# Kernel optimization log

Measured on AMD Instinct MI355X. Metric: run time of the kernel, lower is better.

## Reference

```python
import jax, jax.numpy as jnp
import numpy as np

DIM, HEADS, DH, CHUNK, DEPTH = 1024, 8, 128, 64, 2
BATCH, SEQLEN = 2, 4096
MAX_LR = 0.01
EPS = 1e-6


def _rmsnorm(x, g=None):
    y = x * jax.lax.rsqrt(jnp.mean(x * x, axis=-1, keepdims=True) + EPS)
    return y * g if g is not None else y


def _mem_mlp(ws, x):
    # MemoryMLP: x @ W0, then silu before each subsequent layer
    x = x @ ws[0]
    for w in ws[1:]:
        x = jax.nn.silu(x) @ w
    return x


def _assoc_scan(gates, x):
    # y_t = gates_t * y_{t-1} + x_t along axis 3 (chunk axis)
    g = jnp.broadcast_to(gates, x.shape)
    def op(a, b):
        ga, xa = a
        gb, xb = b
        return ga * gb, gb * xa + xb
    _, y = jax.lax.associative_scan(op, (g, x), axis=3)
    return y


def setup_inputs() -> dict:
    key = jax.random.key(0)
    ks = jax.random.split(key, 12)
    b, n, d, h, dh = BATCH, SEQLEN, DIM, HEADS, DH
    di = h * dh
    lin = lambda k, i, o: jax.random.normal(k, (i, o), jnp.float32) * np.float32(1.0 / np.sqrt(i))
    return {
        "seq": jax.random.normal(ks[0], (b, n, d), jnp.float32),
        "store_norm_g": jnp.ones((d,), jnp.float32),
        "retrieve_norm_g": jnp.ones((d,), jnp.float32),
        "w_kv": lin(ks[1], d, 2 * di),
        "w_q": lin(ks[2], d, di),
        "w_step": lin(ks[3], d, h),
        "w_mom": lin(ks[4], d, h),
        "w_decay": lin(ks[5], d, h),
        "w_gate": lin(ks[6], d, h),
        "w_combine": lin(ks[7], di, d),
        "mh_gamma": jnp.zeros((h, 1, dh), jnp.float32),
        "mem_w0": lin(ks[8], dh, dh),
        "mem_w1": lin(ks[9], dh, dh),
    }


def reference(seq, store_norm_g, retrieve_norm_g, w_kv, w_q, w_step, w_mom,
              w_decay, w_gate, w_combine, mh_gamma, mem_w0, mem_w1):
    b, n, d = seq.shape
    h, dh, c = HEADS, DH, CHUNK
    nc = n // c
    mem_ws = (mem_w0, mem_w1)

    # ---------------- store memories (chunked test-time training) ----------------
    ss = _rmsnorm(seq, store_norm_g)                                    # (b,n,d)
    lr = jax.nn.sigmoid(jnp.einsum('bnd,dh->bhn', ss, w_step)) * MAX_LR  # adaptive step
    lr = lr.reshape(b, h, nc, c)
    cmean = ss.reshape(b, nc, c, d).mean(axis=2)                        # chunk mean-reduce
    mom_gate = jax.nn.sigmoid(jnp.einsum('bnd,dh->bhn', cmean, w_mom))   # (b,h,nc)
    decay = jax.nn.sigmoid(jnp.einsum('bnd,dh->bhn', cmean, w_decay))    # (b,h,nc)

    kv = ss @ w_kv                                                      # (b,n,2*h*dh)
    keys, values = jnp.split(kv, 2, axis=-1)
    split = lambda t: t.reshape(b, n, h, dh).transpose(0, 2, 1, 3).reshape(b, h, nc, c, dh)
    keys, values = split(keys), split(values)

    # per-chunk grad of weighted mse wrt memory MLP weights (vmap(grad), as in torch.func)
    def chunk_loss(ws, k, lrc, v):
        pred = _mem_mlp(ws, k)                                          # (c,dh)
        return jnp.sum(jnp.mean((pred - v) ** 2, axis=-1) * lrc)
    flat = lambda t: t.reshape(b * h * nc, c, dh)
    grads = jax.vmap(jax.grad(chunk_loss), in_axes=(None, 0, 0, 0))(
        mem_ws, flat(keys), lr.reshape(b * h * nc, c), flat(values))
    grads = jnp.stack([g.reshape(b, h, nc, dh, dh) for g in grads])     # (depth,b,h,nc,dh,dh)
    surprise = -grads

    gm = mom_gate[None, :, :, :, None, None]
    gd = (1.0 - decay)[None, :, :, :, None, None]
    momentum = _assoc_scan(gm, surprise)                                # momentum scan over chunks
    updates = _assoc_scan(gd, momentum)                                 # decayed cumulative weight deltas

    # ---------------- retrieve memories ----------------
    sr = _rmsnorm(seq, retrieve_norm_g)
    sr = jnp.pad(sr[:, c - 1:], ((0, 0), (0, c - 1), (0, 0)))           # causal shift by chunk-1
    q = (sr @ w_q).reshape(b, n, h, dh).transpose(0, 2, 1, 3).reshape(b, h, nc, c, dh)

    w0 = mem_w0 + updates[0]                                            # (b,h,nc,dh,dh)
    w1 = mem_w1 + updates[1]
    x = jnp.einsum('bhncd,bhnde->bhnce', q, w0)
    vals = jnp.einsum('bhncd,bhnde->bhnce', jax.nn.silu(x), w1)         # (b,h,nc,c,dh)
    vals = vals.reshape(b, h, n, dh)

    vals = _rmsnorm(vals) * (mh_gamma + 1.0)                            # multihead rmsnorm
    gate = jax.nn.sigmoid(jnp.einsum('bnd,dh->bhn', sr, w_gate))[..., None]
    vals = vals * gate                                                  # retrieve gate (heads>1)
    vals = vals.transpose(0, 2, 1, 3).reshape(b, n, h * dh)             # merge heads
    out = vals @ w_combine                                              # combine heads
    out = jnp.pad(out, ((0, 0), (c - 1, 0), (0, 0)))[:, :n]             # restore alignment
    return out
```

## Files before the change

### kernel.cpp

```cpp
#include <hip/hip_runtime.h>
#include <stdint.h>


#define SEQ 4096
#define NTOK 8192

typedef unsigned short u16;
typedef __attribute__((ext_vector_type(8))) short short8;
typedef __attribute__((ext_vector_type(4))) float f32x4;
typedef __attribute__((ext_vector_type(2))) unsigned int u32x2;

__device__ __forceinline__ u16 f2b(float f) {
  union { float f; uint32_t u; } c; c.f = f;
  uint32_t u = c.u;
  uint32_t r = (u + 0x7fffu + ((u >> 16) & 1u)) >> 16;
  return (u16)r;
}
__device__ __forceinline__ float b2f(u16 h) {
  union { uint32_t u; float f; } c; c.u = ((uint32_t)h) << 16;
  return c.f;
}
__device__ __forceinline__ float sigm(float x) { return 1.f / (1.f + __expf(-x)); }
__device__ __forceinline__ uint32_t pk2(float a, float b) {
  return (uint32_t)f2b(a) | ((uint32_t)f2b(b) << 16);
}
__device__ __forceinline__ void gl16(const void* g, void* l) {
  __builtin_amdgcn_global_load_lds(
      (const __attribute__((address_space(1))) unsigned int*)g,
      (__attribute__((address_space(3))) unsigned int*)l, 16, 0, 0);
}

__device__ __forceinline__ int sidx(int r, int c) {
  return r*128 + ((((c>>3) ^ (r&7))<<3) | (c&7));
}
__device__ __forceinline__ short8 frag_row_lds128(const u16* buf, int row, int ks, int l4) {
  int g = ks*4 + l4;
  return *(const short8*)&buf[row*128 + ((g ^ (row&7))<<3)];
}
__device__ __forceinline__ short8 frag_tile(const u16* t, int row, int ks, int l4) {
  return *(const short8*)&t[row*64 + (((ks*4 + l4) ^ (row&7))<<3)];
}
__device__ __forceinline__ int taddr(int c, int r0) {
  return c*64 + (r0 ^ ((c&7)<<3));
}


__global__ __launch_bounds__(256) void transpose_bf16(
    const float* __restrict__ src, u16* __restrict__ dst, int R, int C)
{
  __shared__ u16 tile[64*66];
  int tiles_x = C >> 6;
  int tx = blockIdx.x % tiles_x, ty = blockIdx.x / tiles_x;
  int c0 = tx*64, r0 = ty*64;
#pragma unroll
  for (int it=0; it<16; ++it) {
    int idx = it*256 + threadIdx.x;
    int rr = idx>>6, cc = idx&63;
    tile[cc*66 + rr] = f2b(src[(size_t)(r0+rr)*C + c0+cc]);
  }
  __syncthreads();
#pragma unroll
  for (int it=0; it<16; ++it) {
    int idx = it*256 + threadIdx.x;
    int rr = idx>>6, cc = idx&63;
    dst[(size_t)(c0+rr)*R + r0+cc] = tile[rr*66 + cc];
  }
}

__global__ __launch_bounds__(256) void smallprep(
    const float* __restrict__ w0, const float* __restrict__ w1,
    u16* __restrict__ w0Ts, u16* __restrict__ w1Ts, u16* __restrict__ w1bs)
{
  int id = blockIdx.x*256 + threadIdx.x;
  int i = id>>7, j = id&127;
  float a = w0[id], b = w1[id];
  w0Ts[sidx(j,i)] = f2b(a);
  w1Ts[sidx(j,i)] = f2b(b);
  w1bs[sidx(i,j)] = f2b(b);
}


__global__ __launch_bounds__(256) void norms_kernel(
    const float* __restrict__ seq, const float* __restrict__ gs,
    const float* __restrict__ gr, const float* __restrict__ wstep,
    const float* __restrict__ wgate, u16* __restrict__ ss,
    u16* __restrict__ sr, float* __restrict__ lr, float* __restrict__ gate)
{
  int t = blockIdx.x; int b = t>>12, pos = t&4095;
  int tid = threadIdx.x;
  const float* row = seq + (size_t)t*1024;
  float x[4]; float ssq = 0.f;
#pragma unroll
  for (int i=0;i<4;++i){ x[i]=row[i*256+tid]; ssq += x[i]*x[i]; }
  for (int m=32;m;m>>=1) ssq += __shfl_xor(ssq, m);
  __shared__ float red[4];
  __shared__ float r2[4][16];
  int wv = tid>>6;
  if ((tid&63)==0) red[wv] = ssq;
  __syncthreads();
  float tot = red[0]+red[1]+red[2]+red[3];
  float inv = rsqrtf(tot*(1.f/1024.f) + 1e-6f);
  float ps[8], pg[8];
#pragma unroll
  for (int h=0;h<8;++h){ ps[h]=0.f; pg[h]=0.f; }
#pragma unroll
  for (int i=0;i<4;++i) {
    int d = i*256+tid;
    float sv = x[i]*inv*gs[d];
    float rv = x[i]*inv*gr[d];
    ss[(size_t)t*1024+d] = f2b(sv);
    sr[(size_t)t*1024+d] = f2b(rv);
#pragma unroll
    for (int h=0;h<8;++h) { ps[h] += sv*wstep[d*8+h]; pg[h] += rv*wgate[d*8+h]; }
  }
#pragma unroll
  for (int h=0;h<8;++h)
    for (int m=32;m;m>>=1){ ps[h] += __shfl_xor(ps[h],m); pg[h] += __shfl_xor(pg[h],m); }
  if ((tid&63)==0) {
#pragma unroll
    for (int h=0;h<8;++h){ r2[wv][h]=ps[h]; r2[wv][8+h]=pg[h]; }
  }
  __syncthreads();
  if (tid < 16) {
    float s = r2[0][tid]+r2[1][tid]+r2[2][tid]+r2[3][tid];
    float sg = sigm(s);
    if (tid<8) lr[((size_t)(b*8+tid))*4096 + pos] = sg*0.01f;
    else gate[((size_t)(b*8+(tid-8)))*4096 + pos] = sg;
  }
}


__global__ __launch_bounds__(256) void chunkgates_kernel(
    const u16* __restrict__ ss, const float* __restrict__ wmom,
    const float* __restrict__ wdec, float* __restrict__ mg,
    float* __restrict__ d1m)
{
  int bc = blockIdx.x; int b = bc>>6, ch = bc&63;
  size_t t0 = (size_t)(b*4096 + ch*64)*1024;
  int tid = threadIdx.x;
  float cm[4]; cm[0]=cm[1]=cm[2]=cm[3]=0.f;
  for (int tok=0; tok<64; ++tok) {
#pragma unroll
    for (int i=0;i<4;++i)
      cm[i] += b2f(ss[t0 + (size_t)tok*1024 + i*256 + tid]);
  }
  float pm[8], pd[8];
#pragma unroll
  for (int h=0;h<8;++h){ pm[h]=0.f; pd[h]=0.f; }
#pragma unroll
  for (int i=0;i<4;++i) {
    float v = cm[i]*(1.f/64.f);
    int d = i*256+tid;
#pragma unroll
    for (int h=0;h<8;++h){ pm[h]+=v*wmom[d*8+h]; pd[h]+=v*wdec[d*8+h]; }
  }
#pragma unroll
  for (int h=0;h<8;++h)
    for (int m=32;m;m>>=1){ pm[h] += __shfl_xor(pm[h],m); pd[h] += __shfl_xor(pd[h],m); }
  __shared__ float r2[4][16];
  int wv = tid>>6;
  if ((tid&63)==0) {
#pragma unroll
    for (int h=0;h<8;++h){ r2[wv][h]=pm[h]; r2[wv][8+h]=pd[h]; }
  }
  __syncthreads();
  if (tid < 16) {
    float s = r2[0][tid]+r2[1][tid]+r2[2][tid]+r2[3][tid];
    if (tid<8) mg[(b*8+tid)*64 + ch] = sigm(s);
    else d1m[(b*8+(tid-8))*64 + ch] = 1.f - sigm(s);
  }
}


__global__ __launch_bounds__(512, 4) void gemm_bt(
    const u16* __restrict__ A, const u16* __restrict__ Bt,
    void* __restrict__ C, int M, int N, int K, int out_f32,
    u16* __restrict__ kvT)
{
  __shared__ __align__(16) u16 As[2][128*64];
  __shared__ __align__(16) u16 Bs[2][128*64];
  int tid = threadIdx.x;
  int w = tid>>6, lane = tid&63;
  int wr = w>>2, wc = w&3;
  int l15 = lane&15, l4 = lane>>4;
  int rl = lane>>3;
  int cg = (lane&7) ^ rl;
  int nwg = gridDim.x*gridDim.y;
  int wg  = blockIdx.y*gridDim.x + blockIdx.x;
  int cpx = nwg >> 3;
  int swz = (wg & 7)*cpx + (wg >> 3);
  int bx = swz % gridDim.x, by = swz / gridDim.x;
  int brow = by*128, bcol = bx*128;
  f32x4 acc[4][2] = {};

  auto STAGE = [&](int buf, int kt) {
#pragma unroll
    for (int i=0;i<2;++i) {
      int row = w*16 + i*8;
      gl16(&A [(size_t)(brow+row+rl)*K + kt + cg*8], &As[buf][row*64]);
      gl16(&Bt[(size_t)(bcol+row+rl)*K + kt + cg*8], &Bs[buf][row*64]);
    }
  };

  int nk = K >> 6;
  STAGE(0, 0);
  asm volatile("s_waitcnt vmcnt(0)");
  __syncthreads();
  for (int t=0; t<nk; ++t) {
    int cur = t & 1;
    if (t+1 < nk) STAGE(cur^1, (t+1)*64);
#pragma unroll
    for (int ks=0; ks<2; ++ks) {
      short8 af[4], bf[2];
#pragma unroll
      for (int m=0;m<4;++m) {
        int row = wr*64 + m*16 + l15;
        int g = ks*4 + l4;
        af[m] = *(const short8*)&As[cur][row*64 + ((g ^ (row&7))<<3)];
      }
#pragma unroll
      for (int n=0;n<2;++n) {
        int row = wc*32 + n*16 + l15;
        int g = ks*4 + l4;
        bf[n] = *(const short8*)&Bs[cur][row*64 + ((g ^ (row&7))<<3)];
      }
#pragma unroll
      for (int m=0;m<4;++m)
#pragma unroll
        for (int n=0;n<2;++n)
          acc[m][n] = __builtin_amdgcn_mfma_f32_16x16x32_bf16(af[m], bf[n], acc[m][n], 0,0,0);
    }
    asm volatile("s_waitcnt vmcnt(0)");
    __syncthreads();
  }
#pragma unroll
  for (int m=0;m<4;++m) {
#pragma unroll
    for (int n=0;n<2;++n) {
      int col = bcol + wc*32 + n*16 + l15;
#pragma unroll
      for (int j=0;j<4;++j) {
        int row = brow + wr*64 + m*16 + l4*4 + j;
        if (out_f32) ((float*)C)[(size_t)row*N + col] = acc[m][n][j];
        else ((u16*)C)[(size_t)row*N + col] = f2b(acc[m][n][j]);
      }
    }
  }
  if (kvT) {
#pragma unroll
    for (int m=0;m<4;++m) {
#pragma unroll
      for (int n=0;n<2;++n) {
        int col = bcol + wc*32 + n*16 + l15;
        if (col < 1024) {
          int row0 = brow + wr*64 + m*16 + l4*4;
          int d = col & 127;
          int chunk = ((row0>>12)*8 + (col>>7))*64 + ((row0&4095)>>6);
          int rr = row0 & 63;
          u32x2 p; p[0] = pk2(acc[m][n][0], acc[m][n][1]);
                   p[1] = pk2(acc[m][n][2], acc[m][n][3]);
          *(u32x2*)&kvT[(size_t)chunk*8192 + taddr(d, rr)] = p;
        }
      }
    }
  }
}


__global__ __launch_bounds__(512) void mlp_fwd(
    const u16* __restrict__ kvout, const float* __restrict__ lr,
    const u16* __restrict__ w0Ts, const u16* __restrict__ w1Ts,
    const u16* __restrict__ w1bs,
    u16* __restrict__ aTg, u16* __restrict__ dpTg, u16* __restrict__ dxTg)
{
  __shared__ __align__(16) u16 W0L[16384];
  __shared__ __align__(16) u16 W1L[16384];
  __shared__ __align__(16) u16 WBL[16384];
  __shared__ __align__(16) u16 abuf[16384];
  int tid = threadIdx.x;
  int w = tid>>6, lane = tid&63;
  int l15 = lane&15, l4 = lane>>4;
#pragma unroll
  for (int it=0; it<4; ++it) {
    int wb = it*512 + w*64;
    gl16((const short8*)w0Ts + wb + lane, (short8*)W0L + wb);
    gl16((const short8*)w1Ts + wb + lane, (short8*)W1L + wb);
    gl16((const short8*)w1bs + wb + lane, (short8*)WBL + wb);
  }
  __syncthreads();
  u16* ab = abuf + w*2048;
  int r0 = l4*4;
  int q = w&3, half = w>>2;
  int rb = q*16;
#pragma unroll
  for (int it2=0; it2<2; ++it2) {
    int cidx = blockIdx.x*4 + it2*2 + half;
    int bh = cidx>>6, ch = cidx&63;
    int b = bh>>3, hh = bh&7;
    size_t t0 = (size_t)(b*4096 + ch*64 + rb);
    size_t tout = (size_t)cidx*8192;
    f32x4 lrv = *(const f32x4*)&lr[(size_t)bh*4096 + ch*64 + rb + r0];

    f32x4 x1[8] = {};
#pragma unroll
    for (int ks=0; ks<4; ++ks) {
      short8 af = *(const short8*)&kvout[(t0 + l15)*2048 + hh*128 + ks*32 + l4*8];
#pragma unroll
      for (int n=0;n<8;++n) {
        short8 bf = frag_row_lds128(W0L, n*16+l15, ks, l4);
        x1[n] = __builtin_amdgcn_mfma_f32_16x16x32_bf16(af, bf, x1[n], 0,0,0);
      }
    }
#pragma unroll
    for (int n=0;n<8;++n) {
      int c = n*16 + l15;
      float av[4];
#pragma unroll
      for (int j=0;j<4;++j){ float xv = x1[n][j]; av[j] = xv*sigm(xv); }
      ab[sidx(r0+0,c)] = f2b(av[0]);
      ab[sidx(r0+1,c)] = f2b(av[1]);
      ab[sidx(r0+2,c)] = f2b(av[2]);
      ab[sidx(r0+3,c)] = f2b(av[3]);
      u32x2 p; p[0] = pk2(av[0],av[1]); p[1] = pk2(av[2],av[3]);
      *(u32x2*)&aTg[tout + taddr(c, rb + r0)] = p;
    }
    f32x4 pr[8] = {};
#pragma unroll
    for (int ks=0; ks<4; ++ks) {
      short8 af = frag_row_lds128(ab, l15, ks, l4);
#pragma unroll
      for (int n=0;n<8;++n) {
        short8 bf = frag_row_lds128(W1L, n*16+l15, ks, l4);
        pr[n] = __builtin_amdgcn_mfma_f32_16x16x32_bf16(af, bf, pr[n], 0,0,0);
      }
    }
#pragma unroll
    for (int n=0;n<8;++n) {
      int c = n*16 + l15;
      float dv[4];
#pragma unroll
      for (int j=0;j<4;++j) {
        float vv = b2f(kvout[(t0+r0+j)*2048 + 1024 + hh*128 + c]);
        dv[j] = 0.015625f * lrv[j] * (pr[n][j] - vv);
      }
      ab[sidx(r0+0,c)] = f2b(dv[0]);
      ab[sidx(r0+1,c)] = f2b(dv[1]);
      ab[sidx(r0+2,c)] = f2b(dv[2]);
      ab[sidx(r0+3,c)] = f2b(dv[3]);
      u32x2 p; p[0] = pk2(dv[0],dv[1]); p[1] = pk2(dv[2],dv[3]);
      *(u32x2*)&dpTg[tout + taddr(c, rb + r0)] = p;
    }
    f32x4 da[8] = {};
#pragma unroll
    for (int ks=0; ks<4; ++ks) {
      short8 af = frag_row_lds128(ab, l15, ks, l4);
#pragma unroll
      for (int n=0;n<8;++n) {
        short8 bf = frag_row_lds128(WBL, n*16+l15, ks, l4);
        da[n] = __builtin_amdgcn_mfma_f32_16x16x32_bf16(af, bf, da[n], 0,0,0);
      }
    }
#pragma unroll
    for (int n=0;n<8;++n) {
      int c = n*16 + l15;
      float d[4];
#pragma unroll
      for (int j=0;j<4;++j) {
        float xv = x1[n][j];
        float sg = sigm(xv);
        d[j] = da[n][j]*(sg*(1.f + xv*(1.f - sg)));
      }
      u32x2 p; p[0] = pk2(d[0],d[1]); p[1] = pk2(d[2],d[3]);
      *(u32x2*)&dxTg[tout + taddr(c, rb + r0)] = p;
    }
  }
}


__global__ __launch_bounds__(256) void grad_op(
    const u16* __restrict__ dpT, const u16* __restrict__ aT,
    const u16* __restrict__ dxT, const u16* __restrict__ kT,
    u16* __restrict__ S)
{
  __shared__ __align__(16) u16 lds[16384];
  int bid = blockIdx.x;
  int op = bid >> 10;
  int sub = bid & 1023, bh = sub>>6, ch = sub&63;
  size_t tin = (size_t)sub*8192;
  const u16* Ain = op ? (dxT + tin) : (dpT + tin);
  const u16* Bin = op ? (kT  + tin) : (aT  + tin);
  int tid = threadIdx.x;
  int w = tid>>6, lane = tid&63;
  int l15 = lane&15, l4 = lane>>4;

#pragma unroll
  for (int it=0; it<4; ++it) {
    int wb = it*256 + w*64;
    gl16((const short8*)Ain + wb + lane, (short8*)lds + wb);
    gl16((const short8*)Bin + wb + lane, (short8*)(lds+8192) + wb);
  }
  __syncthreads();

  f32x4 g[2][8] = {};
#pragma unroll
  for (int ks=0; ks<2; ++ks) {
    short8 af[2];
#pragma unroll
    for (int mi=0; mi<2; ++mi)
      af[mi] = frag_tile(lds, w*32 + mi*16 + l15, ks, l4);
#pragma unroll
    for (int n=0;n<8;++n) {
      short8 bf = frag_tile(lds+8192, n*16 + l15, ks, l4);
#pragma unroll
      for (int mi=0;mi<2;++mi)
        g[mi][n] = __builtin_amdgcn_mfma_f32_16x16x32_bf16(af[mi], bf, g[mi][n], 0,0,0);
    }
  }
  __syncthreads();

#pragma unroll
  for (int mi=0;mi<2;++mi)
#pragma unroll
    for (int n=0;n<8;++n)
#pragma unroll
      for (int j=0;j<4;++j) {
        int m = w*32 + mi*16 + l4*4 + j, c = n*16 + l15;
        lds[sidx(m,c)] = f2b(-g[mi][n][j]);
      }
  __syncthreads();

  u16* Sout = S + ((size_t)((op ? bh : 16+bh))*64 + ch)*16384;
#pragma unroll
  for (int it=0; it<8; ++it)
    ((short8*)Sout)[it*256+tid] = ((const short8*)lds)[it*256+tid];
}


__global__ __launch_bounds__(256) void scan_kernel(
    u16* __restrict__ S, const float* __restrict__ mg, const float* __restrict__ d1m,
    const u16* __restrict__ w0Ts, const u16* __restrict__ w1Ts)
{
  int bidx = blockIdx.x;
  int eblk = bidx & 63;
  int mbh = bidx >> 6;
  int bh = mbh & 15;
  int e = eblk*256 + threadIdx.x;
  u16* base = S + (size_t)mbh*64*16384 + e;
  float wv = b2f(((mbh < 16) ? w0Ts : w1Ts)[e]);
  const float* g1 = mg + bh*64;
  const float* g2 = d1m + bh*64;
  float mom = 0.f, upd = 0.f;
  for (int c2=0; c2<64; ++c2) {
    float s = b2f(base[(size_t)c2*16384]);
    mom = g1[c2]*mom + s;
    upd = g2[c2]*upd + mom;
    base[(size_t)c2*16384] = f2b(wv + upd);
  }
}


__global__ __launch_bounds__(256) void retrieve_kernel(
    const u16* __restrict__ qn, const u16* __restrict__ W,
    const float* __restrict__ gamma, const float* __restrict__ gate,
    u16* __restrict__ vals)
{
  __shared__ __align__(16) u16 W0s[16384];
  __shared__ __align__(16) u16 W1s[16384];
  __shared__ __align__(16) u16 QA[8192];
  int bid = blockIdx.x;
  int bh = bid>>6, ch = bid&63;
  int b = bh>>3, h = bh&7;
  int tid = threadIdx.x;
  int w = tid>>6, lane = tid&63;
  int l15 = lane&15, l4 = lane>>4;
  const u16* W0g = W + ((size_t)bh*64 + ch)*16384;
  const u16* W1g = W + ((size_t)(16+bh)*64 + ch)*16384;
#pragma unroll
  for (int it=0; it<8; ++it) {
    int wb = it*256 + w*64;
    gl16((const short8*)W0g + wb + lane, (short8*)W0s + wb);
    gl16((const short8*)W1g + wb + lane, (short8*)W1s + wb);
  }
  u16* qa = QA + w*2048;
#pragma unroll
  for (int it=0; it<4; ++it) {
    int task = it*64 + lane;
    int rloc = task>>4, g = task&15;
    int posn = ch*64 + w*16 + rloc + 63;
    short8 v;
    if (posn < 4096) v = *(const short8*)&qn[((size_t)(b*4096+posn))*1024 + h*128 + g*8];
    else {
#pragma unroll
      for (int i=0;i<8;++i) v[i]=0;
    }
    *(short8*)&qa[rloc*128 + ((g ^ (rloc&7))<<3)] = v;
  }
  __syncthreads();
  f32x4 xx[8] = {};
#pragma unroll
  for (int ks=0; ks<4; ++ks) {
    short8 af = frag_row_lds128(qa, l15, ks, l4);
#pragma unroll
    for (int n=0;n<8;++n) {
      short8 bf = frag_row_lds128(W0s, n*16+l15, ks, l4);
      xx[n] = __builtin_amdgcn_mfma_f32_16x16x32_bf16(af, bf, xx[n], 0,0,0);
    }
  }
  int r0 = l4*4;
#pragma unroll
  for (int n=0;n<8;++n) {
    int c = n*16 + l15;
#pragma unroll
    for (int j=0;j<4;++j) {
      float xv = xx[n][j];
      qa[sidx(r0+j,c)] = f2b(xv * sigm(xv));
    }
  }
  f32x4 vv[8] = {};
#pragma unroll
  for (int ks=0; ks<4; ++ks) {
    short8 af = frag_row_lds128(qa, l15, ks, l4);
#pragma unroll
    for (int n=0;n<8;++n) {
      short8 bf = frag_row_lds128(W1s, n*16+l15, ks, l4);
      vv[n] = __builtin_amdgcn_mfma_f32_16x16x32_bf16(af, bf, vv[n], 0,0,0);
    }
  }
#pragma unroll
  for (int j=0;j<4;++j) {
    float ssq = 0.f;
#pragma unroll
    for (int n=0;n<8;++n) ssq += vv[n][j]*vv[n][j];
    ssq += __shfl_xor(ssq,1); ssq += __shfl_xor(ssq,2);
    ssq += __shfl_xor(ssq,4); ssq += __shfl_xor(ssq,8);
    float rms = rsqrtf(ssq*(1.f/128.f) + 1e-6f);
    int posn = ch*64 + w*16 + r0 + j + 63;
    if (posn < 4096) {
      float gt = gate[(size_t)bh*4096 + posn];
      size_t orow = ((size_t)(b*4096+posn))*1024 + h*128;
#pragma unroll
      for (int n=0;n<8;++n) {
        int c = n*16 + l15;
        vals[orow + c] = f2b(vv[n][j]*rms*(1.f + gamma[h*128+c])*gt);
      }
    }
  }
}

extern "C" void kernel_launch(void* const* d_in, const int* in_sizes, int n_in,
                              void* d_out, int out_size, void* d_ws, size_t ws_size,
                              hipStream_t stream) {
  const float* seq    = (const float*)d_in[0];
  const float* gstore = (const float*)d_in[1];
  const float* gret   = (const float*)d_in[2];
  const float* wkv    = (const float*)d_in[3];
  const float* wq     = (const float*)d_in[4];
  const float* wstep  = (const float*)d_in[5];
  const float* wmom   = (const float*)d_in[6];
  const float* wdec   = (const float*)d_in[7];
  const float* wgate  = (const float*)d_in[8];
  const float* wcomb  = (const float*)d_in[9];
  const float* gamma  = (const float*)d_in[10];
  const float* w0f    = (const float*)d_in[11];
  const float* w1f    = (const float*)d_in[12];
  float* out = (float*)d_out;
  (void)in_sizes; (void)n_in; (void)out_size; (void)ws_size;

  char* p = (char*)d_ws;
  size_t off = 0;
  auto alloc = [&](size_t bytes) -> void* {
    void* r = p + off; off += (bytes + 255) & ~(size_t)255; return r;
  };
  u16* wkvT   = (u16*)alloc((size_t)2048*1024*2);
  u16* wqT    = (u16*)alloc((size_t)1024*1024*2);
  u16* wcombT = (u16*)alloc((size_t)1024*1024*2);
  u16* w0Ts   = (u16*)alloc(16384*2);
  u16* w1Ts   = (u16*)alloc(16384*2);
  u16* w1bs   = (u16*)alloc(16384*2);
  u16* ss     = (u16*)alloc((size_t)NTOK*1024*2);
  u16* sr     = (u16*)alloc((size_t)NTOK*1024*2);
  u16* kvout  = (u16*)alloc((size_t)NTOK*2048*2);
  u16* qn     = (u16*)alloc((size_t)NTOK*1024*2);
  u16* vals   = (u16*)alloc((size_t)NTOK*1024*2);
  float* lr   = (float*)alloc((size_t)16*4096*4);
  float* gate = (float*)alloc((size_t)16*4096*4);
  float* mg   = (float*)alloc(1024*4);
  float* d1m  = (float*)alloc(1024*4);
  u16* S      = (u16*)alloc((size_t)32*64*16384*2);
  u16* kTg    = (u16*)alloc((size_t)1024*8192*2);
  u16* aTg    = (u16*)alloc((size_t)1024*8192*2);
  u16* dpTg   = (u16*)alloc((size_t)1024*8192*2);
  u16* dxTg   = (u16*)alloc((size_t)1024*8192*2);

  transpose_bf16<<<dim3(512),dim3(256),0,stream>>>(wkv, wkvT, 1024, 2048);
  transpose_bf16<<<dim3(256),dim3(256),0,stream>>>(wq, wqT, 1024, 1024);
  transpose_bf16<<<dim3(256),dim3(256),0,stream>>>(wcomb, wcombT, 1024, 1024);
  smallprep<<<dim3(64),dim3(256),0,stream>>>(w0f, w1f, w0Ts, w1Ts, w1bs);
  norms_kernel<<<dim3(NTOK),dim3(256),0,stream>>>(seq, gstore, gret, wstep, wgate, ss, sr, lr, gate);
  chunkgates_kernel<<<dim3(128),dim3(256),0,stream>>>(ss, wmom, wdec, mg, d1m);
  gemm_bt<<<dim3(16,64),dim3(512),0,stream>>>(ss, wkvT, kvout, 8192, 2048, 1024, 0, kTg);
  gemm_bt<<<dim3(8,64),dim3(512),0,stream>>>(sr, wqT, qn, 8192, 1024, 1024, 0, nullptr);
  mlp_fwd<<<dim3(256),dim3(512),0,stream>>>(kvout, lr, w0Ts, w1Ts, w1bs, aTg, dpTg, dxTg);
  grad_op<<<dim3(2048),dim3(256),0,stream>>>(dpTg, aTg, dxTg, kTg, S);
  scan_kernel<<<dim3(2048),dim3(256),0,stream>>>(S, mg, d1m, w0Ts, w1Ts);
  hipMemsetAsync(vals, 0, 63*1024*2, stream);
  hipMemsetAsync(vals + (size_t)4096*1024, 0, 63*1024*2, stream);
  retrieve_kernel<<<dim3(1024),dim3(256),0,stream>>>(qn, S, gamma, gate, vals);
  gemm_bt<<<dim3(8,64),dim3(512),0,stream>>>(vals, wcombT, out, 8192, 1024, 1024, 1, nullptr);
}
```

Before: 259.0 us.

## Split norms kernel and compute step/gate projections with MFMA

The fused norm+projection kernel is split into three parts. A vectorized per-row RMSNorm assigns one row per wavefront and drops the block syncs. A small prep kernel packs w_step/w_gate into bf16, and an MFMA kernel computes the step and gate logits from the bf16 normalized activations. This removes the scalar 16-way dot products and shuffle reductions from the norm kernel. In exchange it adds two launches, a re-read of ss/sr, and bf16 rounding of the projection inputs.

```diff
diff --git a/kernel.cpp b/kernel.cpp
--- a/kernel.cpp
+++ b/kernel.cpp
@@ -79,53 +79,74 @@
   w1bs[sidx(i,j)] = f2b(b);
 }
 
-
-__global__ __launch_bounds__(256) void norms_kernel(
+__global__ __launch_bounds__(256) void proj_prep(
+    const float* __restrict__ wstep, const float* __restrict__ wgatew,
+    u16* __restrict__ Bt16)
+{
+  int id = blockIdx.x*256 + threadIdx.x;
+  int n = id>>10, k = id&1023;
+  float v = (n < 8) ? wstep[k*8 + n] : wgatew[k*8 + (n-8)];
+  Bt16[id] = f2b(v);
+}
+
+
+__global__ __launch_bounds__(256) void norms_only(
     const float* __restrict__ seq, const float* __restrict__ gs,
-    const float* __restrict__ gr, const float* __restrict__ wstep,
-    const float* __restrict__ wgate, u16* __restrict__ ss,
-    u16* __restrict__ sr, float* __restrict__ lr, float* __restrict__ gate)
-{
-  int t = blockIdx.x; int b = t>>12, pos = t&4095;
-  int tid = threadIdx.x;
+    const float* __restrict__ gr, u16* __restrict__ ss, u16* __restrict__ sr)
+{
+  int w = threadIdx.x>>6, lane = threadIdx.x&63;
+  int t = blockIdx.x*4 + w;
   const float* row = seq + (size_t)t*1024;
-  float x[4]; float ssq = 0.f;
-#pragma unroll
-  for (int i=0;i<4;++i){ x[i]=row[i*256+tid]; ssq += x[i]*x[i]; }
+  f32x4 x[4];
+  float ssq = 0.f;
+#pragma unroll
+  for (int j=0;j<4;++j) {
+    x[j] = *(const f32x4*)&row[j*256 + lane*4];
+    ssq += x[j][0]*x[j][0] + x[j][1]*x[j][1] + x[j][2]*x[j][2] + x[j][3]*x[j][3];
+  }
   for (int m=32;m;m>>=1) ssq += __shfl_xor(ssq, m);
-  __shared__ float red[4];
-  __shared__ float r2[4][16];
-  int wv = tid>>6;
-  if ((tid&63)==0) red[wv] = ssq;
-  __syncthreads();
-  float tot = red[0]+red[1]+red[2]+red[3];
-  float inv = rsqrtf(tot*(1.f/1024.f) + 1e-6f);
-  float ps[8], pg[8];
-#pragma unroll
-  for (int h=0;h<8;++h){ ps[h]=0.f; pg[h]=0.f; }
-#pragma unroll
-  for (int i=0;i<4;++i) {
-    int d = i*256+tid;
-    float sv = x[i]*inv*gs[d];
-    float rv = x[i]*inv*gr[d];
-    ss[(size_t)t*1024+d] = f2b(sv);
-    sr[(size_t)t*1024+d] = f2b(rv);
-#pragma unroll
-    for (int h=0;h<8;++h) { ps[h] += sv*wstep[d*8+h]; pg[h] += rv*wgate[d*8+h]; }
-  }
-#pragma unroll
-  for (int h=0;h<8;++h)
-    for (int m=32;m;m>>=1){ ps[h] += __shfl_xor(ps[h],m); pg[h] += __shfl_xor(pg[h],m); }
-  if ((tid&63)==0) {
-#pragma unroll
-    for (int h=0;h<8;++h){ r2[wv][h]=ps[h]; r2[wv][8+h]=pg[h]; }
-  }
-  __syncthreads();
-  if (tid < 16) {
-    float s = r2[0][tid]+r2[1][tid]+r2[2][tid]+r2[3][tid];
-    float sg = sigm(s);
-    if (tid<8) lr[((size_t)(b*8+tid))*4096 + pos] = sg*0.01f;
-    else gate[((size_t)(b*8+(tid-8)))*4096 + pos] = sg;
+  float inv = rsqrtf(ssq*(1.f/1024.f) + 1e-6f);
+#pragma unroll
+  for (int j=0;j<4;++j) {
+    int d = j*256 + lane*4;
+    f32x4 g4 = *(const f32x4*)&gs[d];
+    f32x4 r4 = *(const f32x4*)&gr[d];
+    u32x2 ps, pr;
+    ps[0] = pk2(x[j][0]*inv*g4[0], x[j][1]*inv*g4[1]);
+    ps[1] = pk2(x[j][2]*inv*g4[2], x[j][3]*inv*g4[3]);
+    pr[0] = pk2(x[j][0]*inv*r4[0], x[j][1]*inv*r4[1]);
+    pr[1] = pk2(x[j][2]*inv*r4[2], x[j][3]*inv*r4[3]);
+    *(u32x2*)&ss[(size_t)t*1024 + d] = ps;
+    *(u32x2*)&sr[(size_t)t*1024 + d] = pr;
+  }
+}
+
+
+__global__ __launch_bounds__(64) void proj_kernel(
+    const u16* __restrict__ ss, const u16* __restrict__ sr,
+    const u16* __restrict__ Bt16, float* __restrict__ lr,
+    float* __restrict__ gate)
+{
+  int lane = threadIdx.x;
+  int l15 = lane&15, l4 = lane>>4;
+  size_t t0 = (size_t)blockIdx.x*16;
+  f32x4 acc1 = {}, acc2 = {};
+#pragma unroll 8
+  for (int ks=0; ks<32; ++ks) {
+    int kof = ks*32 + l4*8;
+    short8 bf = *(const short8*)&Bt16[l15*1024 + kof];
+    short8 as = *(const short8*)&ss[(t0+l15)*1024 + kof];
+    short8 ar = *(const short8*)&sr[(t0+l15)*1024 + kof];
+    acc1 = __builtin_amdgcn_mfma_f32_16x16x32_bf16(as, bf, acc1, 0,0,0);
+    acc2 = __builtin_amdgcn_mfma_f32_16x16x32_bf16(ar, bf, acc2, 0,0,0);
+  }
+  int col = l15;
+#pragma unroll
+  for (int j=0;j<4;++j) {
+    int t = (int)t0 + l4*4 + j;
+    int b = t>>12, pos = t&4095;
+    if (col < 8) lr[((size_t)(b*8+col))*4096 + pos] = sigm(acc1[j])*0.01f;
+    else gate[((size_t)(b*8+(col-8)))*4096 + pos] = sigm(acc2[j]);
   }
 }
 
@@ -558,7 +579,7 @@
   const float* wstep  = (const float*)d_in[5];
   const float* wmom   = (const float*)d_in[6];
   const float* wdec   = (const float*)d_in[7];
-  const float* wgate  = (const float*)d_in[8];
+  const float* wgatew = (const float*)d_in[8];
   const float* wcomb  = (const float*)d_in[9];
   const float* gamma  = (const float*)d_in[10];
   const float* w0f    = (const float*)d_in[11];
@@ -577,6 +598,7 @@
   u16* w0Ts   = (u16*)alloc(16384*2);
   u16* w1Ts   = (u16*)alloc(16384*2);
   u16* w1bs   = (u16*)alloc(16384*2);
+  u16* Bt16   = (u16*)alloc(16384*2);
   u16* ss     = (u16*)alloc((size_t)NTOK*1024*2);
   u16* sr     = (u16*)alloc((size_t)NTOK*1024*2);
   u16* kvout  = (u16*)alloc((size_t)NTOK*2048*2);
@@ -596,7 +618,9 @@
   transpose_bf16<<<dim3(256),dim3(256),0,stream>>>(wq, wqT, 1024, 1024);
   transpose_bf16<<<dim3(256),dim3(256),0,stream>>>(wcomb, wcombT, 1024, 1024);
   smallprep<<<dim3(64),dim3(256),0,stream>>>(w0f, w1f, w0Ts, w1Ts, w1bs);
-  norms_kernel<<<dim3(NTOK),dim3(256),0,stream>>>(seq, gstore, gret, wstep, wgate, ss, sr, lr, gate);
+  proj_prep<<<dim3(64),dim3(256),0,stream>>>(wstep, wgatew, Bt16);
+  norms_only<<<dim3(2048),dim3(256),0,stream>>>(seq, gstore, gret, ss, sr);
+  proj_kernel<<<dim3(512),dim3(64),0,stream>>>(ss, sr, Bt16, lr, gate);
   chunkgates_kernel<<<dim3(128),dim3(256),0,stream>>>(ss, wmom, wdec, mg, d1m);
   gemm_bt<<<dim3(16,64),dim3(512),0,stream>>>(ss, wkvT, kvout, 8192, 2048, 1024, 0, kTg);
   gemm_bt<<<dim3(8,64),dim3(512),0,stream>>>(sr, wqT, qn, 8192, 1024, 1024, 0, nullptr);
```

Measured after the change: 238.6 us. 1.09x faster.
